# Kernel tuning notes

Hardware: AMD Instinct MI355X
Metric: run time of the kernel (lower is better)

## Reference

```python
import jax, jax.numpy as jnp
import numpy as np

DIM = 1024
HEADS = 16
HEAD_DIM = DIM // HEADS
DFF = 4 * DIM
BASE_THETA, K_DOP, K_NOR, K_SERO = 0.5, 0.2, 0.15, 0.1
EPS = 1e-5


def _layernorm(x, g, b):
    mu = jnp.mean(x, axis=-1, keepdims=True)
    var = jnp.var(x, axis=-1, keepdims=True)
    return (x - mu) * jax.lax.rsqrt(var + EPS) * g + b


def setup_inputs() -> dict:
    key = jax.random.key(0)
    ks = jax.random.split(key, 16)
    s = 0.02
    d = {
        'x': jax.random.normal(ks[0], (2, 2048, DIM), dtype=jnp.float32),
        'ln1_g': jnp.ones((DIM,), jnp.float32),
        'ln1_b': jnp.zeros((DIM,), jnp.float32),
        'qkv_w': jax.random.normal(ks[1], (DIM, 3 * DIM), jnp.float32) * s,
        'qkv_b': jnp.zeros((3 * DIM,), jnp.float32),
        'proj_w': jax.random.normal(ks[2], (DIM, DIM), jnp.float32) * s,
        'proj_b': jnp.zeros((DIM,), jnp.float32),
        'kq_w': jax.random.normal(ks[3], (DIM, DIM), jnp.float32) * s,
        'kq_b': jnp.zeros((DIM,), jnp.float32),
        'kk_w': jax.random.normal(ks[4], (DIM, DIM), jnp.float32) * s,
        'kk_b': jnp.zeros((DIM,), jnp.float32),
        'kv_w': jax.random.normal(ks[5], (DIM, DIM), jnp.float32) * s,
        'kv_b': jnp.zeros((DIM,), jnp.float32),
        'ko_w': jax.random.normal(ks[6], (DIM, DIM), jnp.float32) * s,
        'ko_b': jnp.zeros((DIM,), jnp.float32),
        'ln2_g': jnp.ones((DIM,), jnp.float32),
        'ln2_b': jnp.zeros((DIM,), jnp.float32),
        'fc1_w': jax.random.normal(ks[7], (DIM, DFF), jnp.float32) * s,
        'fc1_b': jnp.zeros((DFF,), jnp.float32),
        'fc2_w': jax.random.normal(ks[8], (DFF, DIM), jnp.float32) * s,
        'fc2_b': jnp.zeros((DIM,), jnp.float32),
    }
    return d


def _mha(x, qkv_w, qkv_b, proj_w, proj_b):
    B, N, C = x.shape
    qkv = (x @ qkv_w + qkv_b).reshape(B, N, 3, HEADS, HEAD_DIM)
    q, k, v = qkv[:, :, 0], qkv[:, :, 1], qkv[:, :, 2]  # [B,N,H,Hd]
    scale = HEAD_DIM ** -0.5
    attn = jnp.einsum('bnhd,bmhd->bhnm', q, k) * scale
    attn = jax.nn.softmax(attn, axis=-1)
    out = jnp.einsum('bhnm,bmhd->bnhd', attn, v).reshape(B, N, C)
    return out @ proj_w + proj_b


def _kernel_attn(x, kq_w, kq_b, kk_w, kk_b, kv_w, kv_b, ko_w, ko_b):
    q = x @ kq_w + kq_b
    k = x @ kk_w + kk_b
    v = x @ kv_w + kv_b
    qk = jnp.einsum('bnc,bmc->bnm', q, k)
    theta = (BASE_THETA + K_DOP * jax.nn.sigmoid(qk)
             + K_NOR * jnp.tanh(qk) + K_SERO * jax.nn.relu(qk))
    attn = jax.nn.softmax(theta, axis=-1)
    out = jnp.einsum('bnm,bmc->bnc', attn, v)
    return out @ ko_w + ko_b


def reference(x, ln1_g, ln1_b, qkv_w, qkv_b, proj_w, proj_b,
              kq_w, kq_b, kk_w, kk_b, kv_w, kv_b, ko_w, ko_b,
              ln2_g, ln2_b, fc1_w, fc1_b, fc2_w, fc2_b):
    x = x + _mha(_layernorm(x, ln1_g, ln1_b), qkv_w, qkv_b, proj_w, proj_b)
    x = x + _kernel_attn(x, kq_w, kq_b, kk_w, kk_b, kv_w, kv_b, ko_w, ko_b)
    h = _layernorm(x, ln2_g, ln2_b)
    h = jax.nn.gelu(h @ fc1_w + fc1_b, approximate=False) @ fc2_w + fc2_b
    return x + h
```

## Files before the change

### kernel.cpp

```cpp
#include <hip/hip_runtime.h>
#include <math.h>


#define DIMC   1024
#define NTOK   4096
#define SEQ    2048
#define NHEADS 16
#define DFFC   4096
#define QSCALE 0.125f

typedef unsigned short u16;
typedef __attribute__((ext_vector_type(8))) short s16x8;
typedef __attribute__((ext_vector_type(4))) float f32x4;
#define MFMA16(a,b,c) __builtin_amdgcn_mfma_f32_16x16x32_bf16(a,b,c,0,0,0)

__device__ __forceinline__ float b2f(u16 u){ return __uint_as_float(((unsigned int)u)<<16); }
__device__ __forceinline__ u16 f2b(float f){
  unsigned int u = __float_as_uint(f);
  u += 0x7fffu + ((u>>16)&1u);
  return (u16)(u>>16);
}
__device__ __forceinline__ unsigned int pkbf(float a, float b){
  unsigned int r;
  asm("v_cvt_pk_bf16_f32 %0, %1, %2" : "=v"(r) : "v"(a), "v"(b));
  return r;
}

__device__ __forceinline__ float ldIn(const void* base, long idx, int f32){
  return f32 ? ((const float*)base)[idx] : b2f(((const u16*)base)[idx]);
}
__device__ __forceinline__ float4 ldIn4(const void* base, long idx, int f32){
  if (f32) return *(const float4*)((const float*)base + idx);
  ushort4 u = *(const ushort4*)((const u16*)base + idx);
  return make_float4(b2f(u.x), b2f(u.y), b2f(u.z), b2f(u.w));
}
__device__ __forceinline__ void ld8(const void* base, long idx, int f32, float* v){
  if (f32){
    float4 a = *(const float4*)((const float*)base + idx);
    float4 b = *(const float4*)((const float*)base + idx + 4);
    v[0]=a.x; v[1]=a.y; v[2]=a.z; v[3]=a.w;
    v[4]=b.x; v[5]=b.y; v[6]=b.z; v[7]=b.w;
  } else {
    ushort4 a = *(const ushort4*)((const u16*)base + idx);
    ushort4 b = *(const ushort4*)((const u16*)base + idx + 4);
    v[0]=b2f(a.x); v[1]=b2f(a.y); v[2]=b2f(a.z); v[3]=b2f(a.w);
    v[4]=b2f(b.x); v[5]=b2f(b.y); v[6]=b2f(b.z); v[7]=b2f(b.w);
  }
}
__device__ __forceinline__ void st8(void* base, long idx, int f32, const float* v){
  if (f32){
    *(float4*)((float*)base + idx)     = make_float4(v[0],v[1],v[2],v[3]);
    *(float4*)((float*)base + idx + 4) = make_float4(v[4],v[5],v[6],v[7]);
  } else {
    unsigned int q0 = (unsigned int)f2b(v[0]) | ((unsigned int)f2b(v[1])<<16);
    unsigned int q1 = (unsigned int)f2b(v[2]) | ((unsigned int)f2b(v[3])<<16);
    unsigned int q2 = (unsigned int)f2b(v[4]) | ((unsigned int)f2b(v[5])<<16);
    unsigned int q3 = (unsigned int)f2b(v[6]) | ((unsigned int)f2b(v[7])<<16);
    *(uint4*)((u16*)base + idx) = make_uint4(q0,q1,q2,q3);
  }
}

__device__ __forceinline__ float waveSum(float v){
  #pragma unroll
  for (int off=32; off>0; off>>=1) v += __shfl_xor(v, off, 64);
  return v;
}

__device__ __forceinline__ void async16(const u16* g, u16* l){
  __builtin_amdgcn_global_load_lds(
      (const __attribute__((address_space(1))) unsigned int*)g,
      (__attribute__((address_space(3))) unsigned int*)l, 16, 0, 0);
}

__global__ void detect_kernel(const void* ones, int* flag){
  if (threadIdx.x == 0 && blockIdx.x == 0){
    unsigned int w = *(const unsigned int*)ones;
    *flag = (w == 0x3F803F80u) ? 0 : 1;
  }
}

__global__ __launch_bounds__(256)
void transpose_w(const void* __restrict__ in, u16* __restrict__ out,
                 const int* __restrict__ flagp, int K, int N)
{
  __shared__ u16 t[32][36];
  const int fl = *flagp;
  const int n0 = blockIdx.x*32, k0 = blockIdx.y*32;
  const int tx = threadIdx.x & 31, ty = threadIdx.x >> 5;
  #pragma unroll
  for (int r = ty; r < 32; r += 8)
    t[r][tx] = f2b(ldIn(in, (long)(k0+r)*N + n0 + tx, fl));
  __syncthreads();
  #pragma unroll
  for (int r = ty; r < 32; r += 8)
    out[(long)(n0+r)*K + k0 + tx] = t[tx][r];
}

__global__ __launch_bounds__(256)
void transpose_b(const u16* __restrict__ in, u16* __restrict__ out,
                 int K, int N, long sIn, long sOut)
{
  __shared__ u16 t[32][36];
  const long zi = (long)blockIdx.z*sIn, zo = (long)blockIdx.z*sOut;
  const int n0 = blockIdx.x*32, k0 = blockIdx.y*32;
  const int tx = threadIdx.x & 31, ty = threadIdx.x >> 5;
  #pragma unroll
  for (int r = ty; r < 32; r += 8)
    t[r][tx] = in[zi + (long)(k0+r)*N + n0 + tx];
  __syncthreads();
  #pragma unroll
  for (int r = ty; r < 32; r += 8)
    out[zo + (long)(n0+r)*K + k0 + tx] = t[tx][r];
}

__global__ __launch_bounds__(256)
void conv_bf16(const void* __restrict__ in, u16* __restrict__ out,
               const int* __restrict__ flagp)
{
  const int fl = *flagp;
  long i = ((long)blockIdx.x*256 + threadIdx.x)*4;
  float4 v = ldIn4(in, i, fl);
  ushort4 o; o.x=f2b(v.x); o.y=f2b(v.y); o.z=f2b(v.z); o.w=f2b(v.w);
  *(ushort4*)(out+i) = o;
}

template<int BM, int MODE, int ACT>
__global__ __launch_bounds__(256)
void gemm_mfma(const u16* __restrict__ A, const u16* __restrict__ BT,
               const void* __restrict__ bias, const void* __restrict__ bias2,
               const void* __restrict__ bias3, const void* res,
               void* C, u16* Cv, const int* __restrict__ flagp, int cExt,
               int M, int N, int K, int lda, int ldb, int ldc,
               long sA, long sB, long sC)
{
  constexpr int DEPTH = (BM==128) ? 1 : 3;
  constexpr int BUFS = (BM+128)*64;
  constexpr int ST   = BM*132;
  constexpr int LSZ  = (DEPTH*BUFS > ST) ? DEPTH*BUFS : ST;
  __shared__ u16 lds[LSZ];

  const int fl = *flagp;
  const int fC = cExt ? fl : 0;
  const int z = blockIdx.z;
  A += (long)z*sA; BT += (long)z*sB;
  const long coff = (long)z*sC;
  const int m0 = blockIdx.x*BM, n0 = blockIdx.y*128;
  const int tid = threadIdx.x, w = tid>>6, l = tid&63;
  const int lr = l&15, lq = l>>4;
  constexpr int FM = BM/32;
  constexpr int NIA = BM/32;
  const int wm = (w&1)*(BM/2), wn = (w>>1)*64;

  const int rq = l>>3;
  const int cperm = (l&7) ^ rq;
  const u16* pa = A  + (long)(m0 + rq)*lda + cperm*8;
  const u16* pb = BT + (long)(n0 + rq)*ldb + cperm*8;

  f32x4 acc[FM][4];
  #pragma unroll
  for (int i=0;i<FM;i++)
    #pragma unroll
    for (int j=0;j<4;j++) acc[i][j] = (f32x4){0.f,0.f,0.f,0.f};

  auto stage = [&](u16* buf){
    u16* As = buf;
    u16* Bs = buf + BM*64;
    #pragma unroll
    for (int p=0;p<NIA;p++){
      const int ia = p*4 + w;
      async16(pa + (long)ia*8*lda, &As[ia*512]);
    }
    #pragma unroll
    for (int p=0;p<4;p++){
      const int ib = p*4 + w;
      async16(pb + (long)ib*8*ldb, &Bs[ib*512]);
    }
    pa += 64; pb += 64;
  };

  auto compute = [&](const u16* As){
    const u16* Bs = As + BM*64;
    const int swz = lr & 7;
    #pragma unroll
    for (int h=0; h<2; h++){
      s16x8 af[FM], bf[4];
      const int slot = ((h*4 + lq) ^ swz) << 3;
      #pragma unroll
      for (int i=0;i<FM;i++)
        af[i] = *(const s16x8*)&As[(wm + i*16 + lr)*64 + slot];
      #pragma unroll
      for (int j=0;j<4;j++)
        bf[j] = *(const s16x8*)&Bs[(wn + j*16 + lr)*64 + slot];
      __builtin_amdgcn_s_setprio(1);
      #pragma unroll
      for (int i=0;i<FM;i++)
        #pragma unroll
        for (int j=0;j<4;j++) acc[i][j] = MFMA16(af[i], bf[j], acc[i][j]);
      __builtin_amdgcn_s_setprio(0);
    }
  };

  const int nk = K >> 6;

  if constexpr (DEPTH == 3){
    auto waitL = [&](){
      asm volatile("s_waitcnt vmcnt(6)" ::: "memory");
      __builtin_amdgcn_s_barrier();
    };
    stage(lds);
    stage(lds + BUFS);
    int cur = 0;
    for (int t = 0; t < nk-2; ++t){
      waitL();
      int nxt = cur+2; if (nxt >= 3) nxt -= 3;
      stage(lds + nxt*BUFS);
      compute(lds + cur*BUFS);
      cur = (cur==2) ? 0 : cur+1;
    }
    waitL();
    compute(lds + cur*BUFS);
    cur = (cur==2) ? 0 : cur+1;
    asm volatile("s_waitcnt vmcnt(0)" ::: "memory");
    __builtin_amdgcn_s_barrier();
    compute(lds + cur*BUFS);
    __syncthreads();
  } else {
    for (int t = 0; t < nk; ++t){
      stage(lds);
      asm volatile("s_waitcnt vmcnt(0)" ::: "memory");
      __builtin_amdgcn_s_barrier();
      compute(lds);
      __syncthreads();
    }
  }

  #pragma unroll
  for (int i=0;i<FM;i++)
    #pragma unroll
    for (int j=0;j<4;j++)
      #pragma unroll
      for (int r=0;r<4;r++)
        lds[(wm + i*16 + lq*4 + r)*132 + wn + j*16 + lr] = f2b(acc[i][j][r]);
  __syncthreads();

  const int trow = tid >> 4, tcol = (tid & 15)*8;
  const int gcol = n0 + tcol;
  #pragma unroll
  for (int p=0; p<BM/16; p++){
    const int row = p*16 + trow;
    const long grow = m0 + row;
    float v[8];
    #pragma unroll
    for (int e=0;e<8;e++) v[e] = b2f(lds[row*132 + tcol + e]);

    if (MODE == 2){
      #pragma unroll
      for (int e=0;e<8;e++){
        float q = v[e];
        float sig = 1.f/(1.f+__expf(-q));
        float th  = 1.f - 2.f/(__expf(2.f*q)+1.f);
        v[e] = __expf(0.5f + 0.2f*sig + 0.15f*th + 0.1f*fmaxf(q,0.f));
      }
      st8(C, coff + grow*ldc + gcol, 0, v);
    } else if (MODE == 1){
      if (n0 < 2048){
        const void* bb = (n0 < 1024) ? bias : bias2;
        const int cofs = (n0 < 1024) ? 0 : 1024;
        float bv[8]; ld8(bb, gcol - cofs, fl, bv);
        #pragma unroll
        for (int e=0;e<8;e++) v[e] += bv[e];
        st8(C, grow*2048 + gcol, 0, v);
      } else {
        float bv[8]; ld8(bias3, gcol - 2048, fl, bv);
        #pragma unroll
        for (int e=0;e<8;e++) v[e] += bv[e];
        st8(Cv, grow*1024 + (gcol - 2048), 0, v);
      }
    } else {
      if (bias){
        float bv[8]; ld8(bias, gcol, fl, bv);
        #pragma unroll
        for (int e=0;e<8;e++) v[e] += bv[e];
      }
      if (MODE == 3 && gcol < 1024){
        #pragma unroll
        for (int e=0;e<8;e++) v[e] *= QSCALE;
      }
      if (ACT==1){
        #pragma unroll
        for (int e=0;e<8;e++){
          float u = v[e];
          float y = 1.5957691216f*u*(1.f + 0.044715f*u*u);
          v[e] = u / (1.f + __expf(-y));
        }
      }
      const long idx = coff + grow*ldc + gcol;
      if (res){
        float rv[8]; ld8(res, idx, fl, rv);
        #pragma unroll
        for (int e=0;e<8;e++) v[e] += rv[e];
      }
      st8(C, idx, fC, v);
    }
  }
}

__global__ __launch_bounds__(256)
void ln_kernel(const void* __restrict__ in, const void* __restrict__ g,
               const void* __restrict__ b, u16* __restrict__ outp,
               const int* __restrict__ flagp, int inFlagged)
{
  const int fl = *flagp;
  const int fin = inFlagged ? fl : 0;
  const int row = blockIdx.x;
  const int tid = threadIdx.x;
  float4 xv = ldIn4(in, (long)row*DIMC + tid*4, fin);
  float v0=xv.x, v1=xv.y, v2=xv.z, v3=xv.w;
  float s  = v0+v1+v2+v3;
  float s2 = v0*v0+v1*v1+v2*v2+v3*v3;
  s = waveSum(s); s2 = waveSum(s2);
  __shared__ float sh[8];
  int w = tid>>6, ln = tid&63;
  if (ln==0){ sh[w]=s; sh[4+w]=s2; }
  __syncthreads();
  float ts  = sh[0]+sh[1]+sh[2]+sh[3];
  float ts2 = sh[4]+sh[5]+sh[6]+sh[7];
  float mu  = ts * (1.f/1024.f);
  float var = ts2 * (1.f/1024.f) - mu*mu;
  float rs  = rsqrtf(var + 1e-5f);
  int c = tid*4;
  float4 gv = ldIn4(g, c, fl);
  float4 bv = ldIn4(b, c, fl);
  ushort4 o;
  o.x = f2b((v0-mu)*rs*gv.x + bv.x);
  o.y = f2b((v1-mu)*rs*gv.y + bv.y);
  o.z = f2b((v2-mu)*rs*gv.z + bv.z);
  o.w = f2b((v3-mu)*rs*gv.w + bv.w);
  *(ushort4*)(outp + (long)row*DIMC + c) = o;
}

__global__ __launch_bounds__(256)
void mha_flash(const u16* __restrict__ qkv, u16* __restrict__ outp)
{
  __shared__ u16 Kl[64][72];
  __shared__ u16 Vt[64][72];
  __shared__ u16 Pl[4][16][72];
  const int h  = blockIdx.y;
  const int bb = blockIdx.z;
  const int q0 = blockIdx.x * 64;
  const int tid = threadIdx.x, lane = tid & 63, w = tid >> 6;
  const int lr = lane & 15, lq = lane >> 4;
  const long tokBase = (long)bb * SEQ;

  s16x8 qf0, qf1;
  {
    const u16* qp = qkv + (tokBase + q0 + w*16 + lr)*3072 + h*64 + lq*8;
    qf0 = *(const s16x8*)qp;
    qf1 = *(const s16x8*)(qp + 32);
  }
  f32x4 o[4];
  #pragma unroll
  for (int d=0;d<4;d++) o[d] = (f32x4){0.f,0.f,0.f,0.f};
  f32x4 osum = (f32x4){0.f,0.f,0.f,0.f};
  const s16x8 onesv = (s16x8){0x3F80,0x3F80,0x3F80,0x3F80,0x3F80,0x3F80,0x3F80,0x3F80};

  const int p2 = tid & 31, dg = tid >> 5;
  const int kk = tid >> 3, kd = (tid & 7) * 8;

  uint4 kr0, kr1;
  ushort4 va0, va1, vb0, vb1;
  const u16* kbase = qkv + (tokBase + kk)*3072 + 1024 + h*64 + kd;
  const u16* vbase = qkv + (tokBase + 2*p2)*3072 + 2048 + h*64 + dg*8;

  auto ldKV = [&](int k0){
    const u16* kp = kbase + (long)k0*3072;
    kr0 = *(const uint4*)kp;
    kr1 = *(const uint4*)(kp + 32*3072);
    const u16* vp = vbase + (long)k0*3072;
    va0 = *(const ushort4*)vp;          va1 = *(const ushort4*)(vp+4);
    vb0 = *(const ushort4*)(vp+3072);   vb1 = *(const ushort4*)(vp+3076);
  };
  auto wrKV = [&](){
    *(uint4*)&Kl[kk][kd]      = kr0;
    *(uint4*)&Kl[32+kk][kd]   = kr1;
    unsigned int pk;
    #pragma unroll
    for (int jj=0;jj<4;jj++){
      pk = ((const u16*)&va0)[jj] | ((unsigned int)((const u16*)&vb0)[jj] << 16);
      *(unsigned int*)&Vt[dg*8+jj][2*p2] = pk;
      pk = ((const u16*)&va1)[jj] | ((unsigned int)((const u16*)&vb1)[jj] << 16);
      *(unsigned int*)&Vt[dg*8+4+jj][2*p2] = pk;
    }
  };

  ldKV(0);
  for (int k0 = 0; k0 < SEQ; k0 += 64){
    __syncthreads();
    wrKV();
    if (k0 + 64 < SEQ) ldKV(k0 + 64);
    __syncthreads();

    f32x4 s[4];
    #pragma unroll
    for (int c=0;c<4;c++){
      s[c] = (f32x4){0.f,0.f,0.f,0.f};
      s16x8 kf0 = *(const s16x8*)&Kl[c*16+lr][lq*8];
      s16x8 kf1 = *(const s16x8*)&Kl[c*16+lr][lq*8+32];
      __builtin_amdgcn_s_setprio(1);
      s[c] = MFMA16(qf0, kf0, s[c]);
      s[c] = MFMA16(qf1, kf1, s[c]);
      __builtin_amdgcn_s_setprio(0);
    }
    #pragma unroll
    for (int c=0;c<4;c++){
      float p0 = __expf(s[c][0]);
      float p1 = __expf(s[c][1]);
      float p2v = __expf(s[c][2]);
      float p3 = __expf(s[c][3]);
      unsigned int a01 = pkbf(p0, p1);
      unsigned int a23 = pkbf(p2v, p3);
      u16* pr = &Pl[w][lq*4][c*16+lr];
      pr[0]   = (u16)a01;
      pr[72]  = (u16)(a01>>16);
      pr[144] = (u16)a23;
      pr[216] = (u16)(a23>>16);
    }
    s16x8 pf0 = *(const s16x8*)&Pl[w][lr][lq*8];
    s16x8 pf1 = *(const s16x8*)&Pl[w][lr][32+lq*8];
    __builtin_amdgcn_s_setprio(1);
    osum = MFMA16(pf0, onesv, osum);
    osum = MFMA16(pf1, onesv, osum);
    __builtin_amdgcn_s_setprio(0);
    #pragma unroll
    for (int d=0;d<4;d++){
      s16x8 vf0 = *(const s16x8*)&Vt[d*16+lr][lq*8];
      s16x8 vf1 = *(const s16x8*)&Vt[d*16+lr][32+lq*8];
      __builtin_amdgcn_s_setprio(1);
      o[d] = MFMA16(pf0, vf0, o[d]);
      o[d] = MFMA16(pf1, vf1, o[d]);
      __builtin_amdgcn_s_setprio(0);
    }
  }

  #pragma unroll
  for (int r=0;r<4;r++){
    float inv = 1.f / osum[r];
    long row = (tokBase + q0 + w*16 + lq*4 + r) * (long)DIMC + h*64;
    unsigned int pk01 = pkbf(o[0][r]*inv, o[1][r]*inv);
    unsigned int pk23 = pkbf(o[2][r]*inv, o[3][r]*inv);
    outp[row + lr     ] = (u16)pk01;
    outp[row + lr + 16] = (u16)(pk01>>16);
    outp[row + lr + 32] = (u16)pk23;
    outp[row + lr + 48] = (u16)(pk23>>16);
  }
}

__global__ __launch_bounds__(256)
void norm_kernel(const u16* __restrict__ S, u16* __restrict__ kout)
{
  const int row = blockIdx.x;
  const int tid = threadIdx.x;
  const u16* Sr = S + (long)(row>>11)*4194304 + (long)(row&2047)*2048;
  ushort4 u0 = *(const ushort4*)(Sr + tid*8);
  ushort4 u1 = *(const ushort4*)(Sr + tid*8 + 4);
  float s = b2f(u0.x)+b2f(u0.y)+b2f(u0.z)+b2f(u0.w)
          + b2f(u1.x)+b2f(u1.y)+b2f(u1.z)+b2f(u1.w);
  s = waveSum(s);
  __shared__ float sh[4];
  int w = tid>>6, ln = tid&63;
  if (ln==0) sh[w]=s;
  __syncthreads();
  float inv = 1.f/(sh[0]+sh[1]+sh[2]+sh[3]);
  u16* orow = kout + (long)row*DIMC;
  ushort4 v = *(ushort4*)(orow + tid*4);
  v.x = f2b(b2f(v.x)*inv); v.y = f2b(b2f(v.y)*inv);
  v.z = f2b(b2f(v.z)*inv); v.w = f2b(b2f(v.w)*inv);
  *(ushort4*)(orow + tid*4) = v;
}

extern "C" void kernel_launch(void* const* d_in, const int* in_sizes, int n_in,
                              void* d_out, int out_size, void* d_ws, size_t ws_size,
                              hipStream_t stream)
{
  const void* x      = d_in[0];
  const void* ln1_g  = d_in[1];
  const void* ln1_b  = d_in[2];
  const void* qkv_w  = d_in[3];
  const void* qkv_b  = d_in[4];
  const void* proj_w = d_in[5];
  const void* proj_b = d_in[6];
  const void* kq_w   = d_in[7];
  const void* kq_b   = d_in[8];
  const void* kk_w   = d_in[9];
  const void* kk_b   = d_in[10];
  const void* kv_w   = d_in[11];
  const void* kv_b   = d_in[12];
  const void* ko_w   = d_in[13];
  const void* ko_b   = d_in[14];
  const void* ln2_g  = d_in[15];
  const void* ln2_b  = d_in[16];
  const void* fc1_w  = d_in[17];
  const void* fc1_b  = d_in[18];
  const void* fc2_w  = d_in[19];
  const void* fc2_b  = d_in[20];

  int* flag = (int*)d_ws;
  u16* Ar   = (u16*)((char*)d_ws + 64);
  u16* B0   = Ar + 4194304L;
  u16* QK   = B0;
  u16* Vt   = B0 + 8388608L;
  u16* C0   = B0 + 12582912L;
  u16* Sb   = C0;
  u16* WT   = C0;
  u16* vtmp = C0 + 4194304L;
  u16* WT2  = C0 + 4194304L;
  u16* FC1  = B0;
  u16* Qr   = B0;

  dim3 blk(256);
  const void* np = nullptr;

  detect_kernel<<<1, 64, 0, stream>>>(ln1_g, flag);
  transpose_w<<<dim3(96,32), blk, 0, stream>>>(qkv_w, WT, flag, DIMC, 3*DIMC);
  ln_kernel<<<NTOK, blk, 0, stream>>>(x, ln1_g, ln1_b, Ar, flag, 1);
  gemm_mfma<128,3,0><<<dim3(32,24,1), blk, 0, stream>>>(
      Ar, WT, qkv_b, np, np, np, Qr, nullptr, flag, 0,
      NTOK, 3*DIMC, DIMC, DIMC, DIMC, 3*DIMC, 0,0,0);
  mha_flash<<<dim3(SEQ/64, NHEADS, 2), blk, 0, stream>>>(Qr, Ar);
  transpose_w<<<dim3(32,32), blk, 0, stream>>>(proj_w, WT, flag, DIMC, DIMC);
  gemm_mfma<64,0,0><<<dim3(64,8,1), blk, 0, stream>>>(
      Ar, WT, proj_b, np, np, x, d_out, nullptr, flag, 1,
      NTOK, DIMC, DIMC, DIMC, DIMC, DIMC, 0,0,0);
  conv_bf16<<<NTOK, blk, 0, stream>>>(d_out, Ar, flag);
  transpose_w<<<dim3(32,32), blk, 0, stream>>>(kq_w, WT,            flag, DIMC, DIMC);
  transpose_w<<<dim3(32,32), blk, 0, stream>>>(kk_w, WT + 1048576L, flag, DIMC, DIMC);
  transpose_w<<<dim3(32,32), blk, 0, stream>>>(kv_w, WT + 2097152L, flag, DIMC, DIMC);
  gemm_mfma<128,1,0><<<dim3(32,24,1), blk, 0, stream>>>(
      Ar, WT, kq_b, kk_b, kv_b, np, QK, vtmp, flag, 0,
      NTOK, 3*DIMC, DIMC, DIMC, DIMC, 2048, 0,0,0);
  transpose_b<<<dim3(32,64,2), blk, 0, stream>>>(
      vtmp, Vt, SEQ, DIMC, 2097152L, 2097152L);
  gemm_mfma<128,2,0><<<dim3(16,16,2), blk, 0, stream>>>(
      QK, QK + 1024, np, np, np, np, Sb, nullptr, flag, 0,
      SEQ, SEQ, DIMC, 2048, 2048, SEQ, 4194304L, 4194304L, 4194304L);
  gemm_mfma<64,0,0><<<dim3(32,8,2), blk, 0, stream>>>(
      Sb, Vt, np, np, np, np, Ar, nullptr, flag, 0,
      SEQ, DIMC, SEQ, SEQ, SEQ, DIMC, 4194304L, 2097152L, 2097152L);
  norm_kernel<<<NTOK, blk, 0, stream>>>(Sb, Ar);
  transpose_w<<<dim3(32,32), blk, 0, stream>>>(ko_w, WT, flag, DIMC, DIMC);
  gemm_mfma<64,0,0><<<dim3(64,8,1), blk, 0, stream>>>(
      Ar, WT, ko_b, np, np, d_out, d_out, nullptr, flag, 1,
      NTOK, DIMC, DIMC, DIMC, DIMC, DIMC, 0,0,0);
  ln_kernel<<<NTOK, blk, 0, stream>>>(d_out, ln2_g, ln2_b, Ar, flag, 1);
  transpose_w<<<dim3(128,32), blk, 0, stream>>>(fc1_w, WT2, flag, DIMC, DFFC);
  gemm_mfma<128,0,1><<<dim3(32,32,1), blk, 0, stream>>>(
      Ar, WT2, fc1_b, np, np, np, FC1, nullptr, flag, 0,
      NTOK, DFFC, DIMC, DIMC, DIMC, DFFC, 0,0,0);
  transpose_w<<<dim3(32,128), blk, 0, stream>>>(fc2_w, WT2, flag, DFFC, DIMC);
  gemm_mfma<64,0,0><<<dim3(64,8,1), blk, 0, stream>>>(
      FC1, WT2, fc2_b, np, np, d_out, d_out, nullptr, flag, 1,
      NTOK, DIMC, DFFC, DFFC, DFFC, DIMC, 0,0,0);
}
```

Baseline: 609.1 us.

## Fuse softmax row-sum into PV GEMM, enlarge flash tile, batch weight transposes

```diff
diff --git a/kernel.cpp b/kernel.cpp
--- a/kernel.cpp
+++ b/kernel.cpp
@@ -97,6 +97,25 @@
 }
 
 __global__ __launch_bounds__(256)
+void transpose_w3(const void* in0, const void* in1, const void* in2,
+                  u16* __restrict__ out, const int* __restrict__ flagp)
+{
+  __shared__ u16 t[32][36];
+  const int fl = *flagp;
+  const void* in = (blockIdx.z==0) ? in0 : ((blockIdx.z==1) ? in1 : in2);
+  u16* o = out + (long)blockIdx.z*1048576L;
+  const int n0 = blockIdx.x*32, k0 = blockIdx.y*32;
+  const int tx = threadIdx.x & 31, ty = threadIdx.x >> 5;
+  #pragma unroll
+  for (int r = ty; r < 32; r += 8)
+    t[r][tx] = f2b(ldIn(in, (long)(k0+r)*1024 + n0 + tx, fl));
+  __syncthreads();
+  #pragma unroll
+  for (int r = ty; r < 32; r += 8)
+    o[(long)(n0+r)*1024 + k0 + tx] = t[tx][r];
+}
+
+__global__ __launch_bounds__(256)
 void transpose_b(const u16* __restrict__ in, u16* __restrict__ out,
                  int K, int N, long sIn, long sOut)
 {
@@ -157,10 +176,13 @@
   const u16* pb = BT + (long)(n0 + rq)*ldb + cperm*8;
 
   f32x4 acc[FM][4];
-  #pragma unroll
-  for (int i=0;i<FM;i++)
+  f32x4 osum[FM];
+  #pragma unroll
+  for (int i=0;i<FM;i++){
+    osum[i] = (f32x4){0.f,0.f,0.f,0.f};
     #pragma unroll
     for (int j=0;j<4;j++) acc[i][j] = (f32x4){0.f,0.f,0.f,0.f};
+  }
 
   auto stage = [&](u16* buf){
     u16* As = buf;
@@ -196,6 +218,12 @@
       for (int i=0;i<FM;i++)
         #pragma unroll
         for (int j=0;j<4;j++) acc[i][j] = MFMA16(af[i], bf[j], acc[i][j]);
+      if constexpr (MODE==5){
+        const s16x8 onesv = (s16x8){0x3F80,0x3F80,0x3F80,0x3F80,
+                                    0x3F80,0x3F80,0x3F80,0x3F80};
+        #pragma unroll
+        for (int i=0;i<FM;i++) osum[i] = MFMA16(af[i], onesv, osum[i]);
+      }
       __builtin_amdgcn_s_setprio(0);
     }
   };
@@ -232,6 +260,17 @@
       compute(lds);
       __syncthreads();
     }
+  }
+
+  if constexpr (MODE==5){
+    #pragma unroll
+    for (int i=0;i<FM;i++)
+      #pragma unroll
+      for (int r=0;r<4;r++){
+        float inv = 1.f / osum[i][r];
+        #pragma unroll
+        for (int j=0;j<4;j++) acc[i][j][r] *= inv;
+      }
   }
 
   #pragma unroll
@@ -339,15 +378,15 @@
   *(ushort4*)(outp + (long)row*DIMC + c) = o;
 }
 
-__global__ __launch_bounds__(256)
+__global__ __launch_bounds__(512)
 void mha_flash(const u16* __restrict__ qkv, u16* __restrict__ outp)
 {
   __shared__ u16 Kl[64][72];
   __shared__ u16 Vt[64][72];
-  __shared__ u16 Pl[4][16][72];
+  __shared__ u16 Pl[8][16][72];
   const int h  = blockIdx.y;
   const int bb = blockIdx.z;
-  const int q0 = blockIdx.x * 64;
+  const int q0 = blockIdx.x * 128;
   const int tid = threadIdx.x, lane = tid & 63, w = tid >> 6;
   const int lr = lane & 15, lq = lane >> 4;
   const long tokBase = (long)bb * SEQ;
@@ -364,32 +403,33 @@
   f32x4 osum = (f32x4){0.f,0.f,0.f,0.f};
   const s16x8 onesv = (s16x8){0x3F80,0x3F80,0x3F80,0x3F80,0x3F80,0x3F80,0x3F80,0x3F80};
 
-  const int p2 = tid & 31, dg = tid >> 5;
   const int kk = tid >> 3, kd = (tid & 7) * 8;
-
-  uint4 kr0, kr1;
-  ushort4 va0, va1, vb0, vb1;
+  const bool doV = (tid < 256);
+  const int p2 = tid & 31, dg = (tid >> 5) & 7;
+
+  uint4 kr, vA, vB;
   const u16* kbase = qkv + (tokBase + kk)*3072 + 1024 + h*64 + kd;
   const u16* vbase = qkv + (tokBase + 2*p2)*3072 + 2048 + h*64 + dg*8;
 
   auto ldKV = [&](int k0){
-    const u16* kp = kbase + (long)k0*3072;
-    kr0 = *(const uint4*)kp;
-    kr1 = *(const uint4*)(kp + 32*3072);
-    const u16* vp = vbase + (long)k0*3072;
-    va0 = *(const ushort4*)vp;          va1 = *(const ushort4*)(vp+4);
-    vb0 = *(const ushort4*)(vp+3072);   vb1 = *(const ushort4*)(vp+3076);
+    kr = *(const uint4*)(kbase + (long)k0*3072);
+    if (doV){
+      const u16* vp = vbase + (long)k0*3072;
+      vA = *(const uint4*)vp;
+      vB = *(const uint4*)(vp + 3072);
+    }
   };
   auto wrKV = [&](){
-    *(uint4*)&Kl[kk][kd]      = kr0;
-    *(uint4*)&Kl[32+kk][kd]   = kr1;
-    unsigned int pk;
-    #pragma unroll
-    for (int jj=0;jj<4;jj++){
-      pk = ((const u16*)&va0)[jj] | ((unsigned int)((const u16*)&vb0)[jj] << 16);
-      *(unsigned int*)&Vt[dg*8+jj][2*p2] = pk;
-      pk = ((const u16*)&va1)[jj] | ((unsigned int)((const u16*)&vb1)[jj] << 16);
-      *(unsigned int*)&Vt[dg*8+4+jj][2*p2] = pk;
+    *(uint4*)&Kl[kk][kd] = kr;
+    if (doV){
+      unsigned int pk;
+      #pragma unroll
+      for (int jj=0;jj<4;jj++){
+        pk = ((const u16*)&vA)[jj] | ((unsigned int)((const u16*)&vB)[jj] << 16);
+        *(unsigned int*)&Vt[dg*8+jj][2*p2] = pk;
+        pk = ((const u16*)&vA)[4+jj] | ((unsigned int)((const u16*)&vB)[4+jj] << 16);
+        *(unsigned int*)&Vt[dg*8+4+jj][2*p2] = pk;
+      }
     }
   };
 
@@ -453,29 +493,6 @@
     outp[row + lr + 32] = (u16)pk23;
     outp[row + lr + 48] = (u16)(pk23>>16);
   }
-}
-
-__global__ __launch_bounds__(256)
-void norm_kernel(const u16* __restrict__ S, u16* __restrict__ kout)
-{
-  const int row = blockIdx.x;
-  const int tid = threadIdx.x;
-  const u16* Sr = S + (long)(row>>11)*4194304 + (long)(row&2047)*2048;
-  ushort4 u0 = *(const ushort4*)(Sr + tid*8);
-  ushort4 u1 = *(const ushort4*)(Sr + tid*8 + 4);
-  float s = b2f(u0.x)+b2f(u0.y)+b2f(u0.z)+b2f(u0.w)
-          + b2f(u1.x)+b2f(u1.y)+b2f(u1.z)+b2f(u1.w);
-  s = waveSum(s);
-  __shared__ float sh[4];
-  int w = tid>>6, ln = tid&63;
-  if (ln==0) sh[w]=s;
-  __syncthreads();
-  float inv = 1.f/(sh[0]+sh[1]+sh[2]+sh[3]);
-  u16* orow = kout + (long)row*DIMC;
-  ushort4 v = *(ushort4*)(orow + tid*4);
-  v.x = f2b(b2f(v.x)*inv); v.y = f2b(b2f(v.y)*inv);
-  v.z = f2b(b2f(v.z)*inv); v.w = f2b(b2f(v.w)*inv);
-  *(ushort4*)(orow + tid*4) = v;
 }
 
 extern "C" void kernel_launch(void* const* d_in, const int* in_sizes, int n_in,
@@ -526,15 +543,13 @@
   gemm_mfma<128,3,0><<<dim3(32,24,1), blk, 0, stream>>>(
       Ar, WT, qkv_b, np, np, np, Qr, nullptr, flag, 0,
       NTOK, 3*DIMC, DIMC, DIMC, DIMC, 3*DIMC, 0,0,0);
-  mha_flash<<<dim3(SEQ/64, NHEADS, 2), blk, 0, stream>>>(Qr, Ar);
+  mha_flash<<<dim3(SEQ/128, NHEADS, 2), dim3(512), 0, stream>>>(Qr, Ar);
   transpose_w<<<dim3(32,32), blk, 0, stream>>>(proj_w, WT, flag, DIMC, DIMC);
   gemm_mfma<64,0,0><<<dim3(64,8,1), blk, 0, stream>>>(
       Ar, WT, proj_b, np, np, x, d_out, nullptr, flag, 1,
       NTOK, DIMC, DIMC, DIMC, DIMC, DIMC, 0,0,0);
   conv_bf16<<<NTOK, blk, 0, stream>>>(d_out, Ar, flag);
-  transpose_w<<<dim3(32,32), blk, 0, stream>>>(kq_w, WT,            flag, DIMC, DIMC);
-  transpose_w<<<dim3(32,32), blk, 0, stream>>>(kk_w, WT + 1048576L, flag, DIMC, DIMC);
-  transpose_w<<<dim3(32,32), blk, 0, stream>>>(kv_w, WT + 2097152L, flag, DIMC, DIMC);
+  transpose_w3<<<dim3(32,32,3), blk, 0, stream>>>(kq_w, kk_w, kv_w, WT, flag);
   gemm_mfma<128,1,0><<<dim3(32,24,1), blk, 0, stream>>>(
       Ar, WT, kq_b, kk_b, kv_b, np, QK, vtmp, flag, 0,
       NTOK, 3*DIMC, DIMC, DIMC, DIMC, 2048, 0,0,0);
@@ -543,10 +558,9 @@
   gemm_mfma<128,2,0><<<dim3(16,16,2), blk, 0, stream>>>(
       QK, QK + 1024, np, np, np, np, Sb, nullptr, flag, 0,
       SEQ, SEQ, DIMC, 2048, 2048, SEQ, 4194304L, 4194304L, 4194304L);
-  gemm_mfma<64,0,0><<<dim3(32,8,2), blk, 0, stream>>>(
+  gemm_mfma<64,5,0><<<dim3(32,8,2), blk, 0, stream>>>(
       Sb, Vt, np, np, np, np, Ar, nullptr, flag, 0,
       SEQ, DIMC, SEQ, SEQ, SEQ, DIMC, 4194304L, 2097152L, 2097152L);
-  norm_kernel<<<NTOK, blk, 0, stream>>>(Sb, Ar);
   transpose_w<<<dim3(32,32), blk, 0, stream>>>(ko_w, WT, flag, DIMC, DIMC);
   gemm_mfma<64,0,0><<<dim3(64,8,1), blk, 0, stream>>>(
       Ar, WT, ko_b, np, np, d_out, d_out, nullptr, flag, 1,
```

New measurement: 597.5 us. No clear change (-1.9%).
